# Kernel tuning notes

Measured on AMD Instinct MI355X. Metric: run time of the kernel, lower is better.

## Reference

```python
import jax, jax.numpy as jnp
import numpy as np

B, E, H = 128, 512, 1024
NEG = -1000000.0


def setup_inputs() -> dict:
    key = jax.random.key(0)
    ks = jax.random.split(key, 10)
    inv = 1.0 / np.sqrt(H)
    return {
        "query": jax.random.normal(ks[0], (B, H), jnp.float32),
        "keys": jax.random.normal(ks[1], (B, E, H), jnp.float32),
        "entity_size": jax.random.randint(ks[2], (B,), 0, E + 1, jnp.int32),
        "mention_score": jax.random.normal(ks[3], (B,), jnp.float32),
        # scorer params (torch Linear(2H->H) then Linear(H->1)), stored transposed
        "W1": jax.random.normal(ks[4], (2 * H, H), jnp.float32) * inv,
        "b1": jnp.zeros((H,), jnp.float32),
        "W2": jax.random.normal(ks[5], (H, 1), jnp.float32) * inv,
        "b2": jnp.zeros((1,), jnp.float32),
        "null_address": jax.random.normal(ks[6], (H,), jnp.float32) * inv,
        "new_address": jax.random.normal(ks[7], (H,), jnp.float32) * inv,
    }


def reference(query, keys, entity_size, mention_score, W1, b1, W2, b2, null_address, new_address):
    b, e, h = keys.shape
    # prepend null address, append new address -> [B, E+2, H]
    null = jnp.broadcast_to(null_address, (b, 1, h))
    new = jnp.broadcast_to(new_address, (b, 1, h))
    keys_full = jnp.concatenate([null, keys, new], axis=1)
    q = jnp.broadcast_to(query[:, None, :], (b, e + 2, h))
    qk = jnp.concatenate([q, keys_full], axis=-1)  # [B, E+2, 2H]
    hid = jax.nn.gelu(jnp.einsum("bsd,dh->bsh", qk, W1) + b1, approximate=False)
    scores = (jnp.einsum("bsh,ho->bso", hid, W2) + b2)[..., 0]  # [B, E+2]
    # mention score with sign flip on the null slot (column 0)
    inv_mask = jnp.ones((e + 2,), scores.dtype).at[0].set(-1.0)
    scores = scores + mention_score[:, None] * inv_mask[None, :]
    # mask out slots entity_size[b]+1 .. E (exclusive of the final 'new' slot)
    idx = jnp.arange(e + 2)
    mask = jnp.where((idx[None, :] >= entity_size[:, None] + 1) & (idx[None, :] <= e), NEG, 0.0).astype(scores.dtype)
    return scores + mask
```

## Files before the change

### kernel.cpp

```cpp
#include <hip/hip_runtime.h>
#include <hip/hip_bf16.h>

#define B_ 128
#define E_ 512
#define H_ 1024
#define S_ 514
#define NEGV -1000000.0f

typedef __attribute__((ext_vector_type(8))) short bf16x8;
typedef __attribute__((ext_vector_type(4))) short s16x4;
typedef __attribute__((ext_vector_type(4))) float f32x4;

__device__ __forceinline__ short f2bf(float f) {
  unsigned u = __builtin_bit_cast(unsigned, f);
  return (short)((u + 0x8000u) >> 16);
}

__device__ __forceinline__ float gelu_f(float x) {
  return 0.5f * x * (1.0f + erff(x * 0.7071067811865475f));
}

__global__ void prep_q1(const float* __restrict__ query, const float* __restrict__ W1,
                        const float* __restrict__ b1, const float* __restrict__ nulla,
                        const float* __restrict__ newa, float* __restrict__ Q1,
                        float* __restrict__ N1, float* __restrict__ A1) {
  __shared__ float vec[H_];
  int bid = blockIdx.x;
  int rowIdx = bid >> 2;
  int h = (bid & 3) * 256 + threadIdx.x;
  const float* src;
  int woff;
  if (rowIdx < B_)      { src = query + (size_t)rowIdx * H_; woff = 0; }
  else if (rowIdx == B_){ src = nulla; woff = H_; }
  else                  { src = newa;  woff = H_; }
  for (int i = threadIdx.x; i < H_; i += 256) vec[i] = src[i];
  __syncthreads();
  float acc = (rowIdx < B_) ? b1[h] : 0.f;
  const float* wp = W1 + (size_t)woff * H_ + h;
  #pragma unroll 8
  for (int d = 0; d < H_; ++d) acc += vec[d] * wp[(size_t)d * H_];
  if (rowIdx < B_)       Q1[rowIdx * H_ + h] = acc;
  else if (rowIdx == B_) N1[h] = acc;
  else                   A1[h] = acc;
}

__global__ void transpose_w1k(const float* __restrict__ W1, short* __restrict__ w1kT) {
  __shared__ float tb[64][65];
  int k0 = (blockIdx.x & 15) * 64;
  int n0 = (blockIdx.x >> 4) * 64;
  int x = threadIdx.x & 63;
  int ty = threadIdx.x >> 6;
  #pragma unroll
  for (int i = 0; i < 16; ++i) {
    int row = i * 4 + ty;
    tb[row][x] = W1[(size_t)(H_ + k0 + row) * H_ + n0 + x];
  }
  __syncthreads();
  #pragma unroll
  for (int i = 0; i < 16; ++i) {
    int row = i * 4 + ty;
    w1kT[(size_t)(n0 + row) * H_ + k0 + x] = f2bf(tb[x][row]);
  }
}

__global__ void finalize_base(const int* __restrict__ es, const float* __restrict__ mention,
                              const float* __restrict__ W2, const float* __restrict__ b2,
                              const float* __restrict__ Q1, const float* __restrict__ N1,
                              const float* __restrict__ A1, float* __restrict__ scores) {
  int b = blockIdx.x;
  int t = threadIdx.x;
  float b2v = b2[0], mv = mention[b];
  int esz = es[b];
  for (int s = t; s < S_; s += 256) {
    float base = b2v + (s == 0 ? -mv : mv);
    if (s >= esz + 1 && s <= E_) base += NEGV;
    scores[b * S_ + s] = base;
  }
  float sum0 = 0.f, sum1 = 0.f;
  for (int h = t; h < H_; h += 256) {
    float q = Q1[b * H_ + h], w = W2[h];
    sum0 += gelu_f(q + N1[h]) * w;
    sum1 += gelu_f(q + A1[h]) * w;
  }
  #pragma unroll
  for (int m = 32; m > 0; m >>= 1) { sum0 += __shfl_xor(sum0, m); sum1 += __shfl_xor(sum1, m); }
  __shared__ float red0[4], red1[4];
  int lanei = t & 63, wdi = t >> 6;
  if (lanei == 0) { red0[wdi] = sum0; red1[wdi] = sum1; }
  __syncthreads();
  if (t == 0) {
    scores[b * S_ + 0]      += red0[0] + red0[1] + red0[2] + red0[3];
    scores[b * S_ + S_ - 1] += red1[0] + red1[1] + red1[2] + red1[3];
  }
}

#define BM 128
#define BN 128
#define BK 64
#define LDT 72

__global__ __launch_bounds__(256, 2) void gemm_epilogue(
    const float* __restrict__ keys, const short* __restrict__ w1kT,
    const float* __restrict__ Q1, const float* __restrict__ W2,
    float* __restrict__ scores) {
  __shared__ short As[BM * LDT];
  __shared__ short Bs[BN * LDT];

  int bid = blockIdx.x;
  int cpx = gridDim.x >> 3;
  bid = (bid & 7) * cpx + (bid >> 3);
  int tileM = bid >> 3;
  int tileN = bid & 7;
  int row0 = tileM * BM;
  int col0 = tileN * BN;

  int t = threadIdx.x;
  int lane = t & 63;
  int wid = t >> 6;
  int wr = wid >> 1, wc = wid & 1;
  int l15 = lane & 15, lHi = lane >> 4;

  int asr = t >> 4;
  int asc = (t & 15) * 4;
  int bsr = t >> 3;
  int bsc = (t & 7) * 8;

  const float* aBase = keys + (size_t)(row0 + asr) * H_ + asc;
  const short* bBase = w1kT + (size_t)(col0 + bsr) * H_ + bsc;

  f32x4 aReg[8];
  bf16x8 bReg[4];
  f32x4 acc[4][4];
  #pragma unroll
  for (int m = 0; m < 4; ++m)
    #pragma unroll
    for (int n = 0; n < 4; ++n) acc[m][n] = (f32x4){0.f, 0.f, 0.f, 0.f};

  #pragma unroll
  for (int p = 0; p < 8; ++p) aReg[p] = *(const f32x4*)(aBase + (size_t)p * 16 * H_);
  #pragma unroll
  for (int p = 0; p < 4; ++p) bReg[p] = *(const bf16x8*)(bBase + (size_t)p * 32 * H_);

  for (int k0 = 0; k0 < H_; k0 += BK) {
    __syncthreads();
    #pragma unroll
    for (int p = 0; p < 8; ++p) {
      s16x4 v;
      #pragma unroll
      for (int j = 0; j < 4; ++j) v[j] = f2bf(aReg[p][j]);
      *(s16x4*)&As[(p * 16 + asr) * LDT + asc] = v;
    }
    #pragma unroll
    for (int p = 0; p < 4; ++p)
      *(bf16x8*)&Bs[(p * 32 + bsr) * LDT + bsc] = bReg[p];
    __syncthreads();
    if (k0 + BK < H_) {
      #pragma unroll
      for (int p = 0; p < 8; ++p) aReg[p] = *(const f32x4*)(aBase + (size_t)p * 16 * H_ + k0 + BK);
      #pragma unroll
      for (int p = 0; p < 4; ++p) bReg[p] = *(const bf16x8*)(bBase + (size_t)p * 32 * H_ + k0 + BK);
    }
    #pragma unroll
    for (int kk = 0; kk < 2; ++kk) {
      bf16x8 af[4], bfv[4];
      #pragma unroll
      for (int m = 0; m < 4; ++m)
        af[m] = *(const bf16x8*)&As[(wr * 64 + m * 16 + l15) * LDT + kk * 32 + lHi * 8];
      #pragma unroll
      for (int n = 0; n < 4; ++n)
        bfv[n] = *(const bf16x8*)&Bs[(wc * 64 + n * 16 + l15) * LDT + kk * 32 + lHi * 8];
      #pragma unroll
      for (int m = 0; m < 4; ++m)
        #pragma unroll
        for (int n = 0; n < 4; ++n)
          acc[m][n] = __builtin_amdgcn_mfma_f32_16x16x32_bf16(af[m], bfv[n], acc[m][n], 0, 0, 0);
    }
  }

  int bIdx = row0 >> 9;
  float q1v[4], w2v[4];
  #pragma unroll
  for (int n = 0; n < 4; ++n) {
    int col = col0 + wc * 64 + n * 16 + l15;
    q1v[n] = Q1[bIdx * H_ + col];
    w2v[n] = W2[col];
  }
  #pragma unroll
  for (int m = 0; m < 4; ++m) {
    float part[4] = {0.f, 0.f, 0.f, 0.f};
    #pragma unroll
    for (int n = 0; n < 4; ++n)
      #pragma unroll
      for (int i = 0; i < 4; ++i)
        part[i] += gelu_f(acc[m][n][i] + q1v[n]) * w2v[n];
    #pragma unroll
    for (int i = 0; i < 4; ++i) {
      float v = part[i];
      v += __shfl_xor(v, 1);
      v += __shfl_xor(v, 2);
      v += __shfl_xor(v, 4);
      v += __shfl_xor(v, 8);
      if (l15 == 0) {
        int row = row0 + wr * 64 + m * 16 + lHi * 4 + i;
        int s = (row & 511) + 1;
        atomicAdd(&scores[bIdx * S_ + s], v);
      }
    }
  }
}

extern "C" void kernel_launch(void* const* d_in, const int* in_sizes, int n_in,
                              void* d_out, int out_size, void* d_ws, size_t ws_size,
                              hipStream_t stream) {
  const float* query   = (const float*)d_in[0];
  const float* keys    = (const float*)d_in[1];
  const int*   esz     = (const int*)d_in[2];
  const float* mention = (const float*)d_in[3];
  const float* W1      = (const float*)d_in[4];
  const float* b1      = (const float*)d_in[5];
  const float* W2      = (const float*)d_in[6];
  const float* b2      = (const float*)d_in[7];
  const float* nulla   = (const float*)d_in[8];
  const float* newa    = (const float*)d_in[9];
  float* scores = (float*)d_out;

  short* w1kT = (short*)d_ws;
  float* Q1   = (float*)((char*)d_ws + (size_t)2 * 1024 * 1024);
  float* N1   = Q1 + (size_t)B_ * H_;
  float* A1   = N1 + H_;

  prep_q1<<<520, 256, 0, stream>>>(query, W1, b1, nulla, newa, Q1, N1, A1);
  transpose_w1k<<<256, 256, 0, stream>>>(W1, w1kT);
  finalize_base<<<B_, 256, 0, stream>>>(esz, mention, W2, b2, Q1, N1, A1, scores);
  gemm_epilogue<<<4096, 256, 0, stream>>>(keys, w1kT, Q1, W2, scores);
}
```

Before: 645.1 us.

## Pre-convert keys to bf16 and stream GEMM tiles via global_load_lds

```diff
diff --git a/kernel.cpp b/kernel.cpp
--- a/kernel.cpp
+++ b/kernel.cpp
@@ -11,6 +11,9 @@
 typedef __attribute__((ext_vector_type(4))) short s16x4;
 typedef __attribute__((ext_vector_type(4))) float f32x4;
 
+typedef __attribute__((address_space(1))) const void* gptr_t;
+typedef __attribute__((address_space(3))) void* lptr_t;
+
 __device__ __forceinline__ short f2bf(float f) {
   unsigned u = __builtin_bit_cast(unsigned, f);
   return (short)((u + 0x8000u) >> 16);
@@ -18,6 +21,19 @@
 
 __device__ __forceinline__ float gelu_f(float x) {
   return 0.5f * x * (1.0f + erff(x * 0.7071067811865475f));
+}
+
+__global__ void convert_keys(const float* __restrict__ in, short* __restrict__ out) {
+  size_t total = (size_t)B_ * E_ * H_;
+  size_t stride = (size_t)gridDim.x * blockDim.x * 8;
+  for (size_t i = ((size_t)blockIdx.x * blockDim.x + threadIdx.x) * 8; i < total; i += stride) {
+    f32x4 a = *(const f32x4*)(in + i);
+    f32x4 b = *(const f32x4*)(in + i + 4);
+    bf16x8 v;
+    v[0] = f2bf(a[0]); v[1] = f2bf(a[1]); v[2] = f2bf(a[2]); v[3] = f2bf(a[3]);
+    v[4] = f2bf(b[0]); v[5] = f2bf(b[1]); v[6] = f2bf(b[2]); v[7] = f2bf(b[3]);
+    *(bf16x8*)(out + i) = v;
+  }
 }
 
 __global__ void prep_q1(const float* __restrict__ query, const float* __restrict__ W1,
@@ -94,12 +110,113 @@
   }
 }
 
+#define GBM 128
+#define GBN 128
+#define GBK 64
+
+__global__ __launch_bounds__(256, 2) void gemm_bf16(
+    const short* __restrict__ A, const short* __restrict__ Bm,
+    const float* __restrict__ Q1, const float* __restrict__ W2,
+    float* __restrict__ scores) {
+  __shared__ short As[GBM * GBK];
+  __shared__ short Bs[GBN * GBK];
+
+  int bid = blockIdx.x;
+  int cpx = gridDim.x >> 3;
+  bid = (bid & 7) * cpx + (bid >> 3);
+  int tileM = bid >> 3;
+  int tileN = bid & 7;
+  int row0 = tileM * GBM;
+  int col0 = tileN * GBN;
+
+  int t = threadIdx.x;
+  int lane = t & 63;
+  int wid = t >> 6;
+  int wr = wid >> 1, wc = wid & 1;
+  int l15 = lane & 15, lHi = lane >> 4;
+
+  int srcRow = lane >> 3;
+  int srcColE = ((lane & 7) ^ (lane >> 3)) << 3;
+  const short* aSrc = A + (size_t)(row0 + wid * 32 + srcRow) * H_ + srcColE;
+  const short* bSrc = Bm + (size_t)(col0 + wid * 32 + srcRow) * H_ + srcColE;
+  short* aDst = As + (wid * 4) * 512;
+  short* bDst = Bs + (wid * 4) * 512;
+
+  f32x4 acc[4][4];
+  #pragma unroll
+  for (int m = 0; m < 4; ++m)
+    #pragma unroll
+    for (int n = 0; n < 4; ++n) acc[m][n] = (f32x4){0.f, 0.f, 0.f, 0.f};
+
+  int swz = (l15 & 7) << 4;
+  const char* aRd = (const char*)As + (wr * 64 + l15) * 128;
+  const char* bRd = (const char*)Bs + (wc * 64 + l15) * 128;
+
+  for (int k0 = 0; k0 < H_; k0 += GBK) {
+    __syncthreads();
+    #pragma unroll
+    for (int i = 0; i < 4; ++i) {
+      __builtin_amdgcn_global_load_lds((gptr_t)(aSrc + (size_t)i * 8 * H_ + k0),
+                                       (lptr_t)(aDst + i * 512), 16, 0, 0);
+      __builtin_amdgcn_global_load_lds((gptr_t)(bSrc + (size_t)i * 8 * H_ + k0),
+                                       (lptr_t)(bDst + i * 512), 16, 0, 0);
+    }
+    __syncthreads();
+    #pragma unroll
+    for (int kk = 0; kk < 2; ++kk) {
+      bf16x8 af[4], bv[4];
+      #pragma unroll
+      for (int m = 0; m < 4; ++m)
+        af[m] = *(const bf16x8*)(aRd + m * 2048 + (((kk << 6) | (lHi << 4)) ^ swz));
+      #pragma unroll
+      for (int n = 0; n < 4; ++n)
+        bv[n] = *(const bf16x8*)(bRd + n * 2048 + (((kk << 6) | (lHi << 4)) ^ swz));
+      #pragma unroll
+      for (int m = 0; m < 4; ++m)
+        #pragma unroll
+        for (int n = 0; n < 4; ++n)
+          acc[m][n] = __builtin_amdgcn_mfma_f32_16x16x32_bf16(af[m], bv[n], acc[m][n], 0, 0, 0);
+    }
+  }
+
+  int bIdx = row0 >> 9;
+  float q1v[4], w2v[4];
+  #pragma unroll
+  for (int n = 0; n < 4; ++n) {
+    int col = col0 + wc * 64 + n * 16 + l15;
+    q1v[n] = Q1[bIdx * H_ + col];
+    w2v[n] = W2[col];
+  }
+  #pragma unroll
+  for (int m = 0; m < 4; ++m) {
+    float part[4] = {0.f, 0.f, 0.f, 0.f};
+    #pragma unroll
+    for (int n = 0; n < 4; ++n)
+      #pragma unroll
+      for (int i = 0; i < 4; ++i)
+        part[i] += gelu_f(acc[m][n][i] + q1v[n]) * w2v[n];
+    #pragma unroll
+    for (int i = 0; i < 4; ++i) {
+      float v = part[i];
+      v += __shfl_xor(v, 1);
+      v += __shfl_xor(v, 2);
+      v += __shfl_xor(v, 4);
+      v += __shfl_xor(v, 8);
+      if (l15 == 0) {
+        int row = row0 + wr * 64 + m * 16 + lHi * 4 + i;
+        int s = (row & 511) + 1;
+        atomicAdd(&scores[bIdx * S_ + s], v);
+      }
+    }
+  }
+}
+
 #define BM 128
 #define BN 128
 #define BK 64
 #define LDT 72
 
-__global__ __launch_bounds__(256, 2) void gemm_epilogue(
+__global__ __launch_bounds__(256, 2) void gemm_f32reg(
     const float* __restrict__ keys, const short* __restrict__ w1kT,
     const float* __restrict__ Q1, const float* __restrict__ W2,
     float* __restrict__ scores) {
@@ -224,13 +341,32 @@
   const float* newa    = (const float*)d_in[9];
   float* scores = (float*)d_out;
 
-  short* w1kT = (short*)d_ws;
-  float* Q1   = (float*)((char*)d_ws + (size_t)2 * 1024 * 1024);
-  float* N1   = Q1 + (size_t)B_ * H_;
-  float* A1   = N1 + H_;
-
-  prep_q1<<<520, 256, 0, stream>>>(query, W1, b1, nulla, newa, Q1, N1, A1);
-  transpose_w1k<<<256, 256, 0, stream>>>(W1, w1kT);
-  finalize_base<<<B_, 256, 0, stream>>>(esz, mention, W2, b2, Q1, N1, A1, scores);
-  gemm_epilogue<<<4096, 256, 0, stream>>>(keys, w1kT, Q1, W2, scores);
-}
+  const size_t keysBfBytes = (size_t)B_ * E_ * H_ * 2;
+  const size_t w1kTBytes   = (size_t)H_ * H_ * 2;
+  const size_t q1Bytes     = (size_t)B_ * H_ * 4;
+  const size_t needPrimary = keysBfBytes + w1kTBytes + q1Bytes + 2 * H_ * 4;
+
+  if (ws_size >= needPrimary) {
+    short* keysBf = (short*)d_ws;
+    short* w1kT   = (short*)((char*)d_ws + keysBfBytes);
+    float* Q1     = (float*)((char*)d_ws + keysBfBytes + w1kTBytes);
+    float* N1     = Q1 + (size_t)B_ * H_;
+    float* A1     = N1 + H_;
+
+    convert_keys<<<8192, 256, 0, stream>>>(keys, keysBf);
+    prep_q1<<<520, 256, 0, stream>>>(query, W1, b1, nulla, newa, Q1, N1, A1);
+    transpose_w1k<<<256, 256, 0, stream>>>(W1, w1kT);
+    finalize_base<<<B_, 256, 0, stream>>>(esz, mention, W2, b2, Q1, N1, A1, scores);
+    gemm_bf16<<<4096, 256, 0, stream>>>(keysBf, w1kT, Q1, W2, scores);
+  } else {
+    short* w1kT = (short*)d_ws;
+    float* Q1   = (float*)((char*)d_ws + w1kTBytes);
+    float* N1   = Q1 + (size_t)B_ * H_;
+    float* A1   = N1 + H_;
+
+    prep_q1<<<520, 256, 0, stream>>>(query, W1, b1, nulla, newa, Q1, N1, A1);
+    transpose_w1k<<<256, 256, 0, stream>>>(W1, w1kT);
+    finalize_base<<<B_, 256, 0, stream>>>(esz, mention, W2, b2, Q1, N1, A1, scores);
+    gemm_f32reg<<<4096, 256, 0, stream>>>(keys, w1kT, Q1, W2, scores);
+  }
+}
```

After: 657.6 us. No clear change (+1.9%).
